# Kernel tuning notes

Hardware: AMD Instinct MI355X
Metric: run time of the kernel (lower is better)

## Reference

```python
import jax, jax.numpy as jnp
import numpy as np

D_MODEL = 1024
NHEAD = 16
HEAD_DIM = D_MODEL // NHEAD
EPS_NORM = 1e-6
EPS_RMS = 1e-6


def setup_inputs() -> dict:
    key = jax.random.key(0)
    ks = jax.random.split(key, 8)
    B, S = 2, 1024
    scale = 1.0 / np.sqrt(D_MODEL)
    x = jax.random.normal(ks[0], (B, S, D_MODEL), dtype=jnp.float32)
    Wq = jax.random.normal(ks[1], (D_MODEL, D_MODEL), dtype=jnp.float32) * scale
    Wk = jax.random.normal(ks[2], (D_MODEL, D_MODEL), dtype=jnp.float32) * scale
    Wv = jax.random.normal(ks[3], (D_MODEL, D_MODEL), dtype=jnp.float32) * scale
    Wb = jax.random.normal(ks[4], (NHEAD, D_MODEL), dtype=jnp.float32) * scale
    Wo = jax.random.normal(ks[5], (D_MODEL, D_MODEL), dtype=jnp.float32) * scale
    rms_w = jnp.ones((D_MODEL,), dtype=jnp.float32)
    return {"x": x, "Wq": Wq, "Wk": Wk, "Wv": Wv, "Wb": Wb, "Wo": Wo, "rms_w": rms_w}


def _l2_normalize(t):
    return t / (jnp.linalg.norm(t, axis=-1, keepdims=True) + EPS_NORM)


def _delta_forward(x, Wq, Wk, Wv, Wb, Wo, rms_w):
    B, S, dm = x.shape
    H, D = NHEAD, HEAD_DIM
    q = _l2_normalize(jax.nn.silu(x @ Wq.T).reshape(B, S, H, D))
    k = _l2_normalize(jax.nn.silu(x @ Wk.T).reshape(B, S, H, D))
    v = jax.nn.silu(x @ Wv.T).reshape(B, S, H, D)
    beta = jax.nn.sigmoid(x @ Wb.T) * 2.0  # (B,S,H), allow_neg_eigval doubles

    # time-major for scan: (S,B,H,D) / (S,B,H)
    qT = q.transpose(1, 0, 2, 3)
    kT = k.transpose(1, 0, 2, 3)
    vT = v.transpose(1, 0, 2, 3)
    bT = beta.transpose(1, 0, 2)

    def step(M, inp):
        qt, kt, vt, bt = inp
        # read state BEFORE update (strictly causal)
        out_t = jnp.einsum('bnh,bnhd->bnd', qt, M)
        retrieved = jnp.einsum('bnhd,bnd->bnh', M, kt)
        delta = vt - retrieved
        M = M + bt[..., None, None] * jnp.einsum('bnh,bnd->bnhd', kt, delta)
        return M, out_t

    M0 = jnp.zeros((B, H, D, D), dtype=x.dtype)
    _, outs = jax.lax.scan(step, M0, (qT, kT, vT, bT))  # (S,B,H,D)
    out = outs.transpose(1, 0, 2, 3).reshape(B, S, dm)

    # RMSNorm
    rms = jnp.sqrt(jnp.mean(out * out, axis=-1, keepdims=True) + EPS_RMS)
    out = out / rms * rms_w
    # output projection (dropout is identity in eval)
    return out @ Wo.T


def reference(x, Wq, Wk, Wv, Wb, Wo, rms_w):
    return _delta_forward(x, Wq, Wk, Wv, Wb, Wo, rms_w)
```

## Files before the change

kernel.cpp:

```cpp
#include <hip/hip_runtime.h>
#include <math.h>

#define D_MODEL 1024
#define NHEAD 16
#define HEAD_DIM 64
#define BATCH 2
#define SEQ 1024
#define ROWS (BATCH * SEQ)
#define RD (ROWS * D_MODEL)
#define WSZ (D_MODEL * D_MODEL)
#define CHUNK 64
#define NCHUNK (SEQ / CHUNK)

typedef __attribute__((ext_vector_type(8))) short bf16x8;
typedef __attribute__((ext_vector_type(8))) unsigned short ushort8;
typedef __attribute__((ext_vector_type(4))) unsigned short us4;
typedef __attribute__((ext_vector_type(4))) float f32x4;
typedef __attribute__((ext_vector_type(4))) unsigned int uint4v;
typedef unsigned short ushort;

__device__ __forceinline__ void load_lds_16u(const unsigned short* g, unsigned short* l) {
    __builtin_amdgcn_global_load_lds((const __attribute__((address_space(1))) void*)g,
                                     (__attribute__((address_space(3))) void*)l, 16, 0, 0);
}
__device__ __forceinline__ unsigned short f2bf(float x) {
    unsigned int u = __float_as_uint(x);
    unsigned int r = (u + 0x7FFFu + ((u >> 16) & 1u)) >> 16;
    return (unsigned short)r;
}
__device__ __forceinline__ float bf2f(unsigned short h) {
    return __uint_as_float(((unsigned int)h) << 16);
}
__device__ __forceinline__ float lane_bcast(float v, int lane) {
    return __uint_as_float(__builtin_amdgcn_readlane(__float_as_uint(v), lane));
}
#define SUBST 512
#define FBUF (8 * SUBST * 2)
__device__ __forceinline__ int fidx(int r, int k) {
    return ((r >> 4) * 2 + (k >> 5)) * SUBST + ((((k & 31) >> 3) << 4) + (r & 15)) * 8 + (k & 7);
}

__global__ __launch_bounds__(256) void split_kernel(const float* __restrict__ X,
                                                    unsigned short* __restrict__ H,
                                                    unsigned short* __restrict__ L,
                                                    int n4) {
    int i = blockIdx.x * 256 + threadIdx.x;
    if (i >= n4) return;
    float4 v = ((const float4*)X)[i];
    us4 h, l;
    h.x = f2bf(v.x); l.x = f2bf(v.x - bf2f(h.x));
    h.y = f2bf(v.y); l.y = f2bf(v.y - bf2f(h.y));
    h.z = f2bf(v.z); l.z = f2bf(v.z - bf2f(h.z));
    h.w = f2bf(v.w); l.w = f2bf(v.w - bf2f(h.w));
    ((us4*)H)[i] = h;
    ((us4*)L)[i] = l;
}

__global__ __launch_bounds__(256) void split3_kernel(const float* __restrict__ W0,
                                                     const float* __restrict__ W1,
                                                     const float* __restrict__ W2,
                                                     unsigned short* __restrict__ H0,
                                                     unsigned short* __restrict__ L0,
                                                     unsigned short* __restrict__ H1,
                                                     unsigned short* __restrict__ L1,
                                                     unsigned short* __restrict__ H2,
                                                     unsigned short* __restrict__ L2) {
    const int n4 = WSZ / 4;
    int i = blockIdx.x * 256 + threadIdx.x;
    const int which = i / n4;
    const int j = i - which * n4;
    const float* X = (which == 0) ? W0 : (which == 1) ? W1 : W2;
    unsigned short* H = (which == 0) ? H0 : (which == 1) ? H1 : H2;
    unsigned short* L = (which == 0) ? L0 : (which == 1) ? L1 : L2;
    float4 v = ((const float4*)X)[j];
    us4 h, l;
    h.x = f2bf(v.x); l.x = f2bf(v.x - bf2f(h.x));
    h.y = f2bf(v.y); l.y = f2bf(v.y - bf2f(h.y));
    h.z = f2bf(v.z); l.z = f2bf(v.z - bf2f(h.z));
    h.w = f2bf(v.w); l.w = f2bf(v.w - bf2f(h.w));
    ((us4*)H)[j] = h;
    ((us4*)L)[j] = l;
}

template <int ACT>
__device__ __forceinline__ void gemm_core(const unsigned short* __restrict__ Ah,
                                          const unsigned short* __restrict__ Al,
                                          const unsigned short* __restrict__ Bh,
                                          const unsigned short* __restrict__ Bl,
                                          float* __restrict__ C,
                                          int M, int N, int K,
                                          unsigned short* LA0, unsigned short* LA1,
                                          unsigned short* LB0, unsigned short* LB1) {
    const int t = threadIdx.x;
    const int wave = t >> 6, lane = t & 63;
    const int wm = wave >> 1, wn = wave & 1;
    const int m16 = lane & 15, kg = lane >> 4;
    const int row0 = blockIdx.y * 128, col0 = blockIdx.x * 64;

    f32x4 acc[4][2];
#pragma unroll
    for (int i = 0; i < 4; ++i)
#pragma unroll
        for (int j = 0; j < 2; ++j) acc[i][j] = (f32x4){0.f, 0.f, 0.f, 0.f};

    for (int k0 = 0; k0 < K; k0 += 32) {
#pragma unroll
        for (int ci = 0; ci < 6; ++ci) {
            const int c = wave * 6 + ci;
            const unsigned short* src;
            unsigned short* dst;
            int g16, rbase;
            if (c < 8)       { src = Ah; dst = &LA0[c * 512];        g16 = c;      rbase = row0; }
            else if (c < 16) { src = Al; dst = &LA1[(c - 8) * 512];  g16 = c - 8;  rbase = row0; }
            else if (c < 20) { src = Bh; dst = &LB0[(c - 16) * 512]; g16 = c - 16; rbase = col0; }
            else             { src = Bl; dst = &LB1[(c - 20) * 512]; g16 = c - 20; rbase = col0; }
            const unsigned short* gp = src + (size_t)(rbase + g16 * 16 + m16) * K + k0 + kg * 8;
            load_lds_16u(gp, dst);
        }
        __syncthreads();

        bf16x8 fah[4], fal[4], fbh[2], fbl[2];
#pragma unroll
        for (int mt = 0; mt < 4; ++mt) {
            const int off = (wm * 4 + mt) * 512 + lane * 8;
            fah[mt] = *(const bf16x8*)&LA0[off];
            fal[mt] = *(const bf16x8*)&LA1[off];
        }
#pragma unroll
        for (int nt = 0; nt < 2; ++nt) {
            const int off = (wn * 2 + nt) * 512 + lane * 8;
            fbh[nt] = *(const bf16x8*)&LB0[off];
            fbl[nt] = *(const bf16x8*)&LB1[off];
        }
#pragma unroll
        for (int mt = 0; mt < 4; ++mt)
#pragma unroll
            for (int nt = 0; nt < 2; ++nt) {
                acc[mt][nt] = __builtin_amdgcn_mfma_f32_16x16x32_bf16(fal[mt], fbh[nt], acc[mt][nt], 0, 0, 0);
                acc[mt][nt] = __builtin_amdgcn_mfma_f32_16x16x32_bf16(fah[mt], fbl[nt], acc[mt][nt], 0, 0, 0);
                acc[mt][nt] = __builtin_amdgcn_mfma_f32_16x16x32_bf16(fah[mt], fbh[nt], acc[mt][nt], 0, 0, 0);
            }
        __syncthreads();
    }

#pragma unroll
    for (int mt = 0; mt < 4; ++mt)
#pragma unroll
        for (int nt = 0; nt < 2; ++nt) {
            const int rowb = row0 + wm * 64 + mt * 16 + kg * 4;
            const int col  = col0 + wn * 32 + nt * 16 + m16;
#pragma unroll
            for (int rg = 0; rg < 4; ++rg) {
                float v = acc[mt][nt][rg];
                if (ACT == 1) v = v / (1.f + expf(-v));
                C[(size_t)(rowb + rg) * N + col] = v;
            }
        }
}

template <int ACT>
__global__ __launch_bounds__(256) void gemm_bf16s(const unsigned short* __restrict__ Ah,
                                                  const unsigned short* __restrict__ Al,
                                                  const unsigned short* __restrict__ Bh,
                                                  const unsigned short* __restrict__ Bl,
                                                  float* __restrict__ C,
                                                  int M, int N, int K) {
    __shared__ unsigned short LA[2][8 * 512];
    __shared__ unsigned short LB[2][4 * 512];
    gemm_core<ACT>(Ah, Al, Bh, Bl, C, M, N, K, LA[0], LA[1], LB[0], LB[1]);
}

__global__ __launch_bounds__(256) void gemm_qkv(const unsigned short* __restrict__ Ah,
                                                const unsigned short* __restrict__ Al,
                                                const unsigned short* __restrict__ Bqh,
                                                const unsigned short* __restrict__ Bql,
                                                const unsigned short* __restrict__ Bkh,
                                                const unsigned short* __restrict__ Bkl,
                                                const unsigned short* __restrict__ Bvh,
                                                const unsigned short* __restrict__ Bvl,
                                                float* __restrict__ Cq,
                                                float* __restrict__ Ck,
                                                float* __restrict__ Cv) {
    __shared__ unsigned short LA[2][8 * 512];
    __shared__ unsigned short LB[2][4 * 512];
    const int z = blockIdx.z;
    const unsigned short* Bh = (z == 0) ? Bqh : (z == 1) ? Bkh : Bvh;
    const unsigned short* Bl = (z == 0) ? Bql : (z == 1) ? Bkl : Bvl;
    float* C = (z == 0) ? Cq : (z == 1) ? Ck : Cv;
    gemm_core<1>(Ah, Al, Bh, Bl, C, ROWS, D_MODEL, D_MODEL, LA[0], LA[1], LB[0], LB[1]);
}

#define LDST 40
template <int ACT>
__global__ __launch_bounds__(256) void gemm_mfma(const float* __restrict__ A,
                                                 const float* __restrict__ B,
                                                 float* __restrict__ C,
                                                 int M, int N, int K) {
    __shared__ unsigned short Ahi[128 * LDST], Alo[128 * LDST];
    __shared__ unsigned short Bhi[128 * LDST], Blo[128 * LDST];

    const int t = threadIdx.x;
    const int wave = t >> 6, lane = t & 63;
    const int wm = wave >> 1, wn = wave & 1;
    const int row0 = blockIdx.y * 128, col0 = blockIdx.x * 128;
    const int sr = t >> 1;
    const int sh = t & 1;
    const int m16 = lane & 15, kg = lane >> 4;

    f32x4 acc[4][4];
#pragma unroll
    for (int i = 0; i < 4; ++i)
#pragma unroll
        for (int j = 0; j < 4; ++j) acc[i][j] = (f32x4){0.f, 0.f, 0.f, 0.f};

    const float* ga = A + (size_t)(row0 + sr) * K + sh * 16;
    const float* gb = B + (size_t)(col0 + sr) * K + sh * 16;
    const int sbase = sr * LDST + sh * 16;

    for (int k0 = 0; k0 < K; k0 += 32) {
        float af[16], bf[16];
#pragma unroll
        for (int i = 0; i < 4; ++i) {
            float4 a4 = *(const float4*)(ga + k0 + i * 4);
            float4 b4 = *(const float4*)(gb + k0 + i * 4);
            af[i * 4 + 0] = a4.x; af[i * 4 + 1] = a4.y; af[i * 4 + 2] = a4.z; af[i * 4 + 3] = a4.w;
            bf[i * 4 + 0] = b4.x; bf[i * 4 + 1] = b4.y; bf[i * 4 + 2] = b4.z; bf[i * 4 + 3] = b4.w;
        }
        ushort8 ah0, ah1, al0, al1, bh0, bh1, bl0, bl1;
#pragma unroll
        for (int j = 0; j < 8; ++j) {
            unsigned short h = f2bf(af[j]);       ah0[j] = h; al0[j] = f2bf(af[j] - bf2f(h));
            h = f2bf(af[j + 8]);                  ah1[j] = h; al1[j] = f2bf(af[j + 8] - bf2f(h));
            h = f2bf(bf[j]);                      bh0[j] = h; bl0[j] = f2bf(bf[j] - bf2f(h));
            h = f2bf(bf[j + 8]);                  bh1[j] = h; bl1[j] = f2bf(bf[j + 8] - bf2f(h));
        }
        *(ushort8*)&Ahi[sbase] = ah0;  *(ushort8*)&Ahi[sbase + 8] = ah1;
        *(ushort8*)&Alo[sbase] = al0;  *(ushort8*)&Alo[sbase + 8] = al1;
        *(ushort8*)&Bhi[sbase] = bh0;  *(ushort8*)&Bhi[sbase + 8] = bh1;
        *(ushort8*)&Blo[sbase] = bl0;  *(ushort8*)&Blo[sbase + 8] = bl1;
        __syncthreads();

        bf16x8 fah[4], fal[4], fbh[4], fbl[4];
#pragma unroll
        for (int i = 0; i < 4; ++i) {
            const int ar = (wm * 64 + i * 16 + m16) * LDST + kg * 8;
            const int br = (wn * 64 + i * 16 + m16) * LDST + kg * 8;
            fah[i] = *(const bf16x8*)&Ahi[ar];
            fal[i] = *(const bf16x8*)&Alo[ar];
            fbh[i] = *(const bf16x8*)&Bhi[br];
            fbl[i] = *(const bf16x8*)&Blo[br];
        }
#pragma unroll
        for (int i = 0; i < 4; ++i)
#pragma unroll
            for (int j = 0; j < 4; ++j) {
                acc[i][j] = __builtin_amdgcn_mfma_f32_16x16x32_bf16(fal[i], fbh[j], acc[i][j], 0, 0, 0);
                acc[i][j] = __builtin_amdgcn_mfma_f32_16x16x32_bf16(fah[i], fbl[j], acc[i][j], 0, 0, 0);
                acc[i][j] = __builtin_amdgcn_mfma_f32_16x16x32_bf16(fah[i], fbh[j], acc[i][j], 0, 0, 0);
            }
        __syncthreads();
    }

#pragma unroll
    for (int i = 0; i < 4; ++i)
#pragma unroll
        for (int j = 0; j < 4; ++j) {
            const int col = col0 + wn * 64 + j * 16 + m16;
            const int rowb = row0 + wm * 64 + i * 16 + kg * 4;
#pragma unroll
            for (int rg = 0; rg < 4; ++rg) {
                float v = acc[i][j][rg];
                if (ACT == 1) v = v / (1.f + expf(-v));
                C[(size_t)(rowb + rg) * N + col] = v;
            }
        }
}

__global__ __launch_bounds__(256) void beta_kernel(const float* __restrict__ x,
                                                   const float* __restrict__ Wb,
                                                   float* __restrict__ beta) {
    const int wave = blockIdx.x * 4 + (threadIdx.x >> 6);
    const int lane = threadIdx.x & 63;
    const float* xr = x + (size_t)wave * D_MODEL;
    float xv[16];
#pragma unroll
    for (int j = 0; j < 16; ++j) xv[j] = xr[lane + 64 * j];
    for (int n = 0; n < NHEAD; ++n) {
        const float* wr = Wb + (size_t)n * D_MODEL;
        float s = 0.f;
#pragma unroll
        for (int j = 0; j < 16; ++j) s += xv[j] * wr[lane + 64 * j];
#pragma unroll
        for (int off = 32; off; off >>= 1) s += __shfl_xor(s, off);
        if (lane == 0) beta[(size_t)wave * NHEAD + n] = 2.f / (1.f + expf(-s));
    }
}

__global__ __launch_bounds__(256) void norm_qk(float* __restrict__ Q,
                                               float* __restrict__ Kp) {
    const int TOT = ROWS * NHEAD;
    int wave = blockIdx.x * 4 + (threadIdx.x >> 6);
    const int lane = threadIdx.x & 63;
    float* T = (wave < TOT) ? Q : Kp;
    int w = (wave < TOT) ? wave : wave - TOT;
    float* p = T + (size_t)(w >> 4) * D_MODEL + (size_t)(w & 15) * HEAD_DIM;
    float v = p[lane];
    float ss = v * v;
#pragma unroll
    for (int off = 32; off; off >>= 1) ss += __shfl_xor(ss, off);
    p[lane] = v / (sqrtf(ss) + 1e-6f);
}

#define SMEM_SCAN 153088

__global__ __launch_bounds__(512, 1) void scan_chunked(const float* __restrict__ Qg,
                                                       const float* __restrict__ Kg,
                                                       const float* __restrict__ Vg,
                                                       const float* __restrict__ Btg,
                                                       float* __restrict__ Yg) {
    extern __shared__ char smem[];
    ushort* Mh_  = (ushort*)(smem + 0 * FBUF);
    ushort* Ml_  = (ushort*)(smem + 1 * FBUF);
    ushort* MTh_ = (ushort*)(smem + 2 * FBUF);
    ushort* MTl_ = (ushort*)(smem + 3 * FBUF);
    ushort* KTh_ = (ushort*)(smem + 4 * FBUF);
    ushort* KTl_ = (ushort*)(smem + 5 * FBUF);
    ushort* V0h_ = (ushort*)(smem + 6 * FBUF);
    ushort* V0l_ = (ushort*)(smem + 7 * FBUF);
    ushort* Gh_  = (ushort*)(smem + 8 * FBUF);
    ushort* Gl_  = (ushort*)(smem + 9 * FBUF);
    ushort* Kh_  = (ushort*)(smem + 10 * FBUF);
    ushort* Kl_  = (ushort*)(smem + 11 * FBUF);
    ushort* DTh_ = Kh_;
    ushort* DTl_ = Kl_;
    ushort* Qh_  = (ushort*)(smem + 12 * FBUF);
    ushort* Ql_  = (ushort*)(smem + 13 * FBUF);
    ushort* Wh_  = Qh_;
    ushort* Wl_  = Ql_;
    float*  V32  = (float*)(smem + 14 * FBUF);
    float*  C032 = V32;
    ushort* Ah_  = (ushort*)(smem + 14 * FBUF + 17408);
    ushort* Al_  = (ushort*)(smem + 15 * FBUF + 17408);
    float*  N32  = (float*)(smem + 16 * FBUF + 17408);
    float*  bv   = (float*)(smem + 16 * FBUF + 17408 + 4352);

    const int b = blockIdx.x >> 4;
    const int n = blockIdx.x & 15;
    const int t = threadIdx.x;
    const int wave = t >> 6, lane = t & 63;
    const int wm = wave >> 1, wn = wave & 1;
    const int m16 = lane & 15, kg = lane >> 4;
    const int bS = b * SEQ;
    const int nOff = n * HEAD_DIM;
    const int r = t >> 3, g = t & 7;

    f32x4 Macc[2], MTacc[2];
#pragma unroll
    for (int j = 0; j < 2; ++j) {
        Macc[j] = (f32x4){0.f, 0.f, 0.f, 0.f};
        MTacc[j] = (f32x4){0.f, 0.f, 0.f, 0.f};
    }

    auto prod_band = [&](const ushort* Ah, const ushort* Al,
                         const ushort* Bh, const ushort* Bl, f32x4 acc[2]) {
        const int lo8 = lane * 8;
#pragma unroll
        for (int half = 0; half < 2; ++half) {
            bf16x8 ah = *(const bf16x8*)&Ah[(wm * 2 + half) * SUBST + lo8];
            bf16x8 al = *(const bf16x8*)&Al[(wm * 2 + half) * SUBST + lo8];
#pragma unroll
            for (int j = 0; j < 2; ++j) {
                const int jg = wn * 2 + j;
                bf16x8 bh = *(const bf16x8*)&Bh[(jg * 2 + half) * SUBST + lo8];
                bf16x8 bl = *(const bf16x8*)&Bl[(jg * 2 + half) * SUBST + lo8];
                acc[j] = __builtin_amdgcn_mfma_f32_16x16x32_bf16(al, bh, acc[j], 0, 0, 0);
                acc[j] = __builtin_amdgcn_mfma_f32_16x16x32_bf16(ah, bl, acc[j], 0, 0, 0);
                acc[j] = __builtin_amdgcn_mfma_f32_16x16x32_bf16(ah, bh, acc[j], 0, 0, 0);
            }
        }
    };

    for (int c = 0; c < NCHUNK; ++c) {
        const int s0 = c * CHUNK;

        {
            const float* gK = Kg + (size_t)(bS + s0 + r) * D_MODEL + nOff + g * 8;
            const float* gQ = Qg + (size_t)(bS + s0 + r) * D_MODEL + nOff + g * 8;
            const float* gV = Vg + (size_t)(bS + s0 + r) * D_MODEL + nOff + g * 8;
            float kf[8], qf[8];
            ushort khv[8], klv[8];
            float4 kv0 = ((const float4*)gK)[0], kv1 = ((const float4*)gK)[1];
            float4 qv0 = ((const float4*)gQ)[0], qv1 = ((const float4*)gQ)[1];
            float4 vv0 = ((const float4*)gV)[0], vv1 = ((const float4*)gV)[1];
            kf[0] = kv0.x; kf[1] = kv0.y; kf[2] = kv0.z; kf[3] = kv0.w;
            kf[4] = kv1.x; kf[5] = kv1.y; kf[6] = kv1.z; kf[7] = kv1.w;
            qf[0] = qv0.x; qf[1] = qv0.y; qf[2] = qv0.z; qf[3] = qv0.w;
            qf[4] = qv1.x; qf[5] = qv1.y; qf[6] = qv1.z; qf[7] = qv1.w;
            *(float4*)&V32[r * 68 + g * 8] = vv0;
            *(float4*)&V32[r * 68 + g * 8 + 4] = vv1;
            ushort8 kh8, kl8, qh8, ql8;
#pragma unroll
            for (int e = 0; e < 8; ++e) {
                ushort h = f2bf(kf[e]);
                ushort l = f2bf(kf[e] - bf2f(h));
                khv[e] = h; klv[e] = l;
                kh8[e] = h; kl8[e] = l;
                h = f2bf(qf[e]); l = f2bf(qf[e] - bf2f(h));
                qh8[e] = h; ql8[e] = l;
            }
            const int o0 = fidx(r, g * 8);
            *(ushort8*)&Kh_[o0] = kh8;
            *(ushort8*)&Kl_[o0] = kl8;
            *(ushort8*)&Qh_[o0] = qh8;
            *(ushort8*)&Ql_[o0] = ql8;
#pragma unroll
            for (int e = 0; e < 8; ++e) {
                const int ib = fidx(g * 8 + e, r);
                KTh_[ib] = khv[e]; KTl_[ib] = klv[e];
            }
            if (t < 64) bv[t] = Btg[(size_t)(bS + s0 + t) * NHEAD + n];
        }
        __syncthreads();

        f32x4 yacc[2], V0acc[2];
        {
            if (c > 0) {
#pragma unroll
                for (int j = 0; j < 2; ++j) V0acc[j] = (f32x4){0.f, 0.f, 0.f, 0.f};
                prod_band(Kh_, Kl_, Mh_, Ml_, V0acc);
#pragma unroll
                for (int j = 0; j < 2; ++j)
#pragma unroll
                    for (int rg = 0; rg < 4; ++rg) {
                        const int row = wm * 16 + kg * 4 + rg, col = wn * 32 + j * 16 + m16;
                        V0acc[j][rg] = V32[row * 68 + col] - V0acc[j][rg];
                    }
            } else {
#pragma unroll
                for (int j = 0; j < 2; ++j)
#pragma unroll
                    for (int rg = 0; rg < 4; ++rg) {
                        const int row = wm * 16 + kg * 4 + rg, col = wn * 32 + j * 16 + m16;
                        V0acc[j][rg] = V32[row * 68 + col];
                    }
            }
#pragma unroll
            for (int j = 0; j < 2; ++j)
#pragma unroll
                for (int rg = 0; rg < 4; ++rg) {
                    const int row = wm * 16 + kg * 4 + rg, col = wn * 32 + j * 16 + m16;
                    float v0 = V0acc[j][rg];
                    ushort h = f2bf(v0);
                    const int ii = fidx(row, col);
                    V0h_[ii] = h; V0l_[ii] = f2bf(v0 - bf2f(h));
                }
#pragma unroll
            for (int j = 0; j < 2; ++j) yacc[j] = (f32x4){0.f, 0.f, 0.f, 0.f};
            if (c > 0) prod_band(Qh_, Ql_, MTh_, MTl_, yacc);
            f32x4 acc[2];
#pragma unroll
            for (int j = 0; j < 2; ++j) acc[j] = (f32x4){0.f, 0.f, 0.f, 0.f};
            prod_band(Kh_, Kl_, Kh_, Kl_, acc);
#pragma unroll
            for (int j = 0; j < 2; ++j)
#pragma unroll
                for (int rg = 0; rg < 4; ++rg) {
                    const int row = wm * 16 + kg * 4 + rg, col = wn * 32 + j * 16 + m16;
                    float av = acc[j][rg];
                    ushort h = f2bf(av);
                    const int ii = fidx(row, col);
                    Ah_[ii] = h; Al_[ii] = f2bf(av - bf2f(h));
                }
#pragma unroll
            for (int j = 0; j < 2; ++j) acc[j] = (f32x4){0.f, 0.f, 0.f, 0.f};
            prod_band(Qh_, Ql_, Kh_, Kl_, acc);
#pragma unroll
            for (int j = 0; j < 2; ++j)
#pragma unroll
                for (int rg = 0; rg < 4; ++rg) {
                    const int row = wm * 16 + kg * 4 + rg, col = wn * 32 + j * 16 + m16;
                    float gv = (row > col) ? acc[j][rg] : 0.f;
                    ushort h = f2bf(gv);
                    const int ii = fidx(row, col);
                    Gh_[ii] = h; Gl_[ii] = f2bf(gv - bf2f(h));
                }
        }
        __syncthreads();

        {
            f32x4 acc[2];
#pragma unroll
            for (int j = 0; j < 2; ++j) acc[j] = (f32x4){0.f, 0.f, 0.f, 0.f};
            prod_band(Kh_, Kl_, V0h_, V0l_, acc);
#pragma unroll
            for (int j = 0; j < 2; ++j)
#pragma unroll
                for (int rg = 0; rg < 4; ++rg) {
                    const int row = wm * 16 + kg * 4 + rg, col = wn * 32 + j * 16 + m16;
                    C032[row * 65 + col] = acc[j][rg];
                }
            for (int i = t; i < 2 * FBUF / 16; i += 512)
                ((uint4v*)Wh_)[i] = (uint4v){0u, 0u, 0u, 0u};
        }
        __syncthreads();

        if (wave == 0) {
#pragma unroll
            for (int J = 0; J < 4; ++J) {
                float Nreg[16];
                if (J > 0) {
#pragma unroll
                    for (int band = 0; band < 4; ++band) {
                        f32x4 acc1 = (f32x4){0.f, 0.f, 0.f, 0.f};
                        const int lo8 = lane * 8;
#pragma unroll
                        for (int half = 0; half < 2; ++half) {
                            bf16x8 ah = *(const bf16x8*)&Ah_[(band * 2 + half) * SUBST + lo8];
                            bf16x8 al = *(const bf16x8*)&Al_[(band * 2 + half) * SUBST + lo8];
                            bf16x8 bh = *(const bf16x8*)&Wh_[(J * 2 + half) * SUBST + lo8];
                            bf16x8 bl = *(const bf16x8*)&Wl_[(J * 2 + half) * SUBST + lo8];
                            acc1 = __builtin_amdgcn_mfma_f32_16x16x32_bf16(al, bh, acc1, 0, 0, 0);
                            acc1 = __builtin_amdgcn_mfma_f32_16x16x32_bf16(ah, bl, acc1, 0, 0, 0);
                            acc1 = __builtin_amdgcn_mfma_f32_16x16x32_bf16(ah, bh, acc1, 0, 0, 0);
                        }
#pragma unroll
                        for (int rg = 0; rg < 4; ++rg)
                            N32[(band * 16 + kg * 4 + rg) * 17 + m16] = acc1[rg];
                    }
#pragma unroll
                    for (int j = 0; j < 16; ++j) Nreg[j] = N32[lane * 17 + j];
                }

                float Areg[16], CNreg[16];
                {
                    bf16x8 a0 = *(const bf16x8*)&Ah_[fidx(lane, 16 * J)];
                    bf16x8 a1 = *(const bf16x8*)&Ah_[fidx(lane, 16 * J + 8)];
                    bf16x8 b0 = *(const bf16x8*)&Al_[fidx(lane, 16 * J)];
                    bf16x8 b1 = *(const bf16x8*)&Al_[fidx(lane, 16 * J + 8)];
#pragma unroll
                    for (int e = 0; e < 8; ++e) {
                        Areg[e]     = bf2f((ushort)a0[e]) + bf2f((ushort)b0[e]);
                        Areg[e + 8] = bf2f((ushort)a1[e]) + bf2f((ushort)b1[e]);
                    }
#pragma unroll
                    for (int j = 0; j < 16; ++j) CNreg[j] = C032[lane * 65 + 16 * J + j];
                    if (J > 0) {
#pragma unroll
                        for (int j = 0; j < 16; ++j) CNreg[j] += Nreg[j];
                    }
                }
                float bvreg = bv[16 * J + m16];

                float wreg[16];
#pragma unroll
                for (int j = 0; j < 16; ++j) {
                    float sA = CNreg[j], sB = 0.f;
#pragma unroll
                    for (int jj = 0; jj < 16; ++jj) {
                        if (jj < j) {
                            float pr = Areg[jj] * lane_bcast(wreg[jj], 16 * J + j);
                            if (jj & 1) sB += pr; else sA += pr;
                        }
                    }
                    float sum = sA + sB;
                    float beta_s = lane_bcast(bvreg, j);
                    wreg[j] = (lane > 16 * J + j) ? (-beta_s * sum) : 0.f;
                }

                {
                    ushort8 h8[2], l8[2];
#pragma unroll
                    for (int e = 0; e < 16; ++e) {
                        ushort h = f2bf(wreg[e]);
                        h8[e >> 3][e & 7] = h;
                        l8[e >> 3][e & 7] = f2bf(wreg[e] - bf2f(h));
                    }
                    const int o0 = fidx(lane, 16 * J), o1 = fidx(lane, 16 * J + 8);
                    *(ushort8*)&Wh_[o0] = h8[0]; *(ushort8*)&Wh_[o1] = h8[1];
                    *(ushort8*)&Wl_[o0] = l8[0]; *(ushort8*)&Wl_[o1] = l8[1];
                }
            }
        }
        __syncthreads();

        {
            f32x4 acc[2];
#pragma unroll
            for (int j = 0; j < 2; ++j) acc[j] = V0acc[j];
            prod_band(Wh_, Wl_, KTh_, KTl_, acc);
#pragma unroll
            for (int j = 0; j < 2; ++j)
#pragma unroll
                for (int rg = 0; rg < 4; ++rg) {
                    const int row = wm * 16 + kg * 4 + rg, col = wn * 32 + j * 16 + m16;
                    float dv = acc[j][rg] * bv[row];
                    ushort h = f2bf(dv);
                    const int ii = fidx(col, row);
                    DTh_[ii] = h; DTl_[ii] = f2bf(dv - bf2f(h));
                }
        }
        __syncthreads();

        {
            prod_band(Gh_, Gl_, DTh_, DTl_, yacc);
#pragma unroll
            for (int j = 0; j < 2; ++j)
#pragma unroll
                for (int rg = 0; rg < 4; ++rg) {
                    const int row = wm * 16 + kg * 4 + rg, col = wn * 32 + j * 16 + m16;
                    Yg[(size_t)(bS + s0 + row) * D_MODEL + nOff + col] = yacc[j][rg];
                }
            prod_band(KTh_, KTl_, DTh_, DTl_, Macc);
            prod_band(DTh_, DTl_, KTh_, KTl_, MTacc);
            if (c < NCHUNK - 1) {
#pragma unroll
                for (int j = 0; j < 2; ++j)
#pragma unroll
                    for (int rg = 0; rg < 4; ++rg) {
                        const int row = wm * 16 + kg * 4 + rg, col = wn * 32 + j * 16 + m16;
                        const int ii = fidx(row, col);
                        float mv = Macc[j][rg];
                        ushort h = f2bf(mv);
                        Mh_[ii] = h; Ml_[ii] = f2bf(mv - bf2f(h));
                        mv = MTacc[j][rg];
                        h = f2bf(mv);
                        MTh_[ii] = h; MTl_[ii] = f2bf(mv - bf2f(h));
                    }
            }
        }
        __syncthreads();
    }
}

template <int SPLIT>
__global__ __launch_bounds__(256) void rmsnorm_kernel(float* __restrict__ Y,
                                                      const float* __restrict__ w,
                                                      unsigned short* __restrict__ H,
                                                      unsigned short* __restrict__ L) {
    __shared__ float red[4];
    float* y = Y + (size_t)blockIdx.x * D_MODEL;
    const int t = threadIdx.x;
    const int wv = t >> 6, ln = t & 63;
    float4 v = ((float4*)y)[t];
    float ss = v.x * v.x + v.y * v.y + v.z * v.z + v.w * v.w;
#pragma unroll
    for (int off = 32; off; off >>= 1) ss += __shfl_xor(ss, off);
    if (ln == 0) red[wv] = ss;
    __syncthreads();
    float tot = red[0] + red[1] + red[2] + red[3];
    float inv = 1.f / sqrtf(tot * (1.f / D_MODEL) + 1e-6f);
    const float4 wv4 = ((const float4*)w)[t];
    v.x *= inv * wv4.x; v.y *= inv * wv4.y;
    v.z *= inv * wv4.z; v.w *= inv * wv4.w;
    if (SPLIT) {
        us4 h, l;
        h.x = f2bf(v.x); l.x = f2bf(v.x - bf2f(h.x));
        h.y = f2bf(v.y); l.y = f2bf(v.y - bf2f(h.y));
        h.z = f2bf(v.z); l.z = f2bf(v.z - bf2f(h.z));
        h.w = f2bf(v.w); l.w = f2bf(v.w - bf2f(h.w));
        size_t i = (size_t)blockIdx.x * 256 + t;
        ((us4*)H)[i] = h;
        ((us4*)L)[i] = l;
    } else {
        ((float4*)y)[t] = v;
    }
}

extern "C" void kernel_launch(void* const* d_in, const int* in_sizes, int n_in,
                              void* d_out, int out_size, void* d_ws, size_t ws_size,
                              hipStream_t stream) {
    const float* x     = (const float*)d_in[0];
    const float* Wq    = (const float*)d_in[1];
    const float* Wk    = (const float*)d_in[2];
    const float* Wv    = (const float*)d_in[3];
    const float* Wb    = (const float*)d_in[4];
    const float* Wo    = (const float*)d_in[5];
    const float* rms_w = (const float*)d_in[6];
    float* out = (float*)d_out;

    char* p = (char*)d_ws;
    float* Q  = (float*)p;  p += (size_t)RD * 4;
    float* Kp = (float*)p;  p += (size_t)RD * 4;
    float* Vp = (float*)p;  p += (size_t)RD * 4;
    float* Y  = (float*)p;  p += (size_t)RD * 4;
    float* Bt = (float*)p;  p += (size_t)32768 * 4;
    unsigned short* xh  = (unsigned short*)p;  p += (size_t)RD * 2;
    unsigned short* xl  = (unsigned short*)p;  p += (size_t)RD * 2;
    unsigned short* Wsh = (unsigned short*)p;  p += (size_t)WSZ * 2;
    unsigned short* Wsl = (unsigned short*)p;  p += (size_t)WSZ * 2;
    const size_t need_fast = (size_t)RD * 16 + 131072 + (size_t)RD * 4 + (size_t)WSZ * 4;
    const bool fast = ws_size >= need_fast;

    unsigned short* Wkh = (unsigned short*)Y;
    unsigned short* Wkl = Wkh + WSZ;
    unsigned short* Wvh = Wkl + WSZ;
    unsigned short* Wvl = Wvh + WSZ;

    (void)hipFuncSetAttribute(reinterpret_cast<const void*>(scan_chunked),
                              hipFuncAttributeMaxDynamicSharedMemorySize, SMEM_SCAN);

    if (fast) {
        dim3 ggrid(D_MODEL / 64, ROWS / 128);
        dim3 qgrid(D_MODEL / 64, ROWS / 128, 3);
        split_kernel<<<RD / 4 / 256, 256, 0, stream>>>(x, xh, xl, RD / 4);
        split3_kernel<<<3 * WSZ / 4 / 256, 256, 0, stream>>>(Wq, Wk, Wv,
                                                             Wsh, Wsl, Wkh, Wkl, Wvh, Wvl);
        gemm_qkv<<<qgrid, 256, 0, stream>>>(xh, xl, Wsh, Wsl, Wkh, Wkl, Wvh, Wvl,
                                            Q, Kp, Vp);
        beta_kernel<<<ROWS / 4, 256, 0, stream>>>(x, Wb, Bt);
        norm_qk<<<2 * ROWS * NHEAD / 4, 256, 0, stream>>>(Q, Kp);
        scan_chunked<<<BATCH * NHEAD, 512, SMEM_SCAN, stream>>>(Q, Kp, Vp, Bt, Y);
        rmsnorm_kernel<1><<<ROWS, 256, 0, stream>>>(Y, rms_w, xh, xl);
        split_kernel<<<WSZ / 4 / 256, 256, 0, stream>>>(Wo, Wsh, Wsl, WSZ / 4);
        gemm_bf16s<0><<<ggrid, 256, 0, stream>>>(xh, xl, Wsh, Wsl, out, ROWS, D_MODEL, D_MODEL);
    } else {
        dim3 ggrid(D_MODEL / 128, ROWS / 128);
        gemm_mfma<1><<<ggrid, 256, 0, stream>>>(x, Wq, Q, ROWS, D_MODEL, D_MODEL);
        gemm_mfma<1><<<ggrid, 256, 0, stream>>>(x, Wk, Kp, ROWS, D_MODEL, D_MODEL);
        gemm_mfma<1><<<ggrid, 256, 0, stream>>>(x, Wv, Vp, ROWS, D_MODEL, D_MODEL);
        beta_kernel<<<ROWS / 4, 256, 0, stream>>>(x, Wb, Bt);
        norm_qk<<<2 * ROWS * NHEAD / 4, 256, 0, stream>>>(Q, Kp);
        scan_chunked<<<BATCH * NHEAD, 512, SMEM_SCAN, stream>>>(Q, Kp, Vp, Bt, Y);
        rmsnorm_kernel<0><<<ROWS, 256, 0, stream>>>(Y, rms_w, nullptr, nullptr);
        gemm_mfma<0><<<ggrid, 256, 0, stream>>>(Y, Wo, out, ROWS, D_MODEL, D_MODEL);
    }
}
```

Measured before the change: 445.0 us.

## Overlap Q/G products with serial W solve and prefetch next chunk

Restructures the chunked delta-rule scan. Waves 1-7 now compute the Q·M^T and the causal Q·K^T (G) tiles while wave 0 does the serial triangular W solve, skipping G tiles that are entirely masked. The next chunk's K/Q/V are prefetched into registers, beta for the whole sequence is loaded once, and the MT state is written as the transpose of M instead of running a second MFMA product. The K A-fragments are reused across products. The cost is more registers and uneven per-wave work.

```diff
diff --git a/kernel.cpp b/kernel.cpp
--- a/kernel.cpp
+++ b/kernel.cpp
@@ -311,7 +311,7 @@
     p[lane] = v / (sqrtf(ss) + 1e-6f);
 }
 
-#define SMEM_SCAN 153088
+#define SMEM_SCAN 156160
 
 __global__ __launch_bounds__(512, 1) void scan_chunked(const float* __restrict__ Qg,
                                                        const float* __restrict__ Kg,
@@ -327,6 +327,8 @@
     ushort* KTl_ = (ushort*)(smem + 5 * FBUF);
     ushort* V0h_ = (ushort*)(smem + 6 * FBUF);
     ushort* V0l_ = (ushort*)(smem + 7 * FBUF);
+    ushort* Wh_  = V0h_;
+    ushort* Wl_  = V0l_;
     ushort* Gh_  = (ushort*)(smem + 8 * FBUF);
     ushort* Gl_  = (ushort*)(smem + 9 * FBUF);
     ushort* Kh_  = (ushort*)(smem + 10 * FBUF);
@@ -335,14 +337,11 @@
     ushort* DTl_ = Kl_;
     ushort* Qh_  = (ushort*)(smem + 12 * FBUF);
     ushort* Ql_  = (ushort*)(smem + 13 * FBUF);
-    ushort* Wh_  = Qh_;
-    ushort* Wl_  = Ql_;
-    float*  V32  = (float*)(smem + 14 * FBUF);
-    float*  C032 = V32;
-    ushort* Ah_  = (ushort*)(smem + 14 * FBUF + 17408);
-    ushort* Al_  = (ushort*)(smem + 15 * FBUF + 17408);
-    float*  N32  = (float*)(smem + 16 * FBUF + 17408);
-    float*  bv   = (float*)(smem + 16 * FBUF + 17408 + 4352);
+    float*  C032 = (float*)(smem + 14 * FBUF);
+    ushort* Ah_  = (ushort*)(smem + 14 * FBUF + 16640);
+    ushort* Al_  = (ushort*)(smem + 15 * FBUF + 16640);
+    float*  N32  = (float*)(smem + 16 * FBUF + 16640);
+    float*  bAll = (float*)(smem + 16 * FBUF + 16640 + 4352);
 
     const int b = blockIdx.x >> 4;
     const int n = blockIdx.x & 15;
@@ -354,51 +353,62 @@
     const int nOff = n * HEAD_DIM;
     const int r = t >> 3, g = t & 7;
 
-    f32x4 Macc[2], MTacc[2];
-#pragma unroll
-    for (int j = 0; j < 2; ++j) {
-        Macc[j] = (f32x4){0.f, 0.f, 0.f, 0.f};
-        MTacc[j] = (f32x4){0.f, 0.f, 0.f, 0.f};
-    }
-
-    auto prod_band = [&](const ushort* Ah, const ushort* Al,
-                         const ushort* Bh, const ushort* Bl, f32x4 acc[2]) {
+    f32x4 Macc[2];
+    Macc[0] = (f32x4){0.f, 0.f, 0.f, 0.f};
+    Macc[1] = (f32x4){0.f, 0.f, 0.f, 0.f};
+
+    auto load_af = [&](const ushort* Xh, const ushort* Xl, int tm, bf16x8* oh, bf16x8* ol) {
         const int lo8 = lane * 8;
 #pragma unroll
         for (int half = 0; half < 2; ++half) {
-            bf16x8 ah = *(const bf16x8*)&Ah[(wm * 2 + half) * SUBST + lo8];
-            bf16x8 al = *(const bf16x8*)&Al[(wm * 2 + half) * SUBST + lo8];
+            oh[half] = *(const bf16x8*)&Xh[(tm * 2 + half) * SUBST + lo8];
+            ol[half] = *(const bf16x8*)&Xl[(tm * 2 + half) * SUBST + lo8];
+        }
+    };
+    auto prod_cA = [&](const bf16x8* ah, const bf16x8* al,
+                       const ushort* Bh, const ushort* Bl, int tn, f32x4* acc) {
+        const int lo8 = lane * 8;
+#pragma unroll
+        for (int half = 0; half < 2; ++half) {
 #pragma unroll
             for (int j = 0; j < 2; ++j) {
-                const int jg = wn * 2 + j;
+                const int jg = tn * 2 + j;
                 bf16x8 bh = *(const bf16x8*)&Bh[(jg * 2 + half) * SUBST + lo8];
                 bf16x8 bl = *(const bf16x8*)&Bl[(jg * 2 + half) * SUBST + lo8];
-                acc[j] = __builtin_amdgcn_mfma_f32_16x16x32_bf16(al, bh, acc[j], 0, 0, 0);
-                acc[j] = __builtin_amdgcn_mfma_f32_16x16x32_bf16(ah, bl, acc[j], 0, 0, 0);
-                acc[j] = __builtin_amdgcn_mfma_f32_16x16x32_bf16(ah, bh, acc[j], 0, 0, 0);
+                acc[j] = __builtin_amdgcn_mfma_f32_16x16x32_bf16(al[half], bh, acc[j], 0, 0, 0);
+                acc[j] = __builtin_amdgcn_mfma_f32_16x16x32_bf16(ah[half], bl, acc[j], 0, 0, 0);
+                acc[j] = __builtin_amdgcn_mfma_f32_16x16x32_bf16(ah[half], bh, acc[j], 0, 0, 0);
             }
         }
     };
+
+    for (int i = t; i < SEQ; i += 512) bAll[i] = Btg[(size_t)(bS + i) * NHEAD + n];
+
+    float4 pk0, pk1, pq0, pq1;
+    float pv[8];
+    auto issue_pf = [&](int cc) {
+        const int so = cc * CHUNK;
+        const float* gK = Kg + (size_t)(bS + so + r) * D_MODEL + nOff + g * 8;
+        const float* gQ = Qg + (size_t)(bS + so + r) * D_MODEL + nOff + g * 8;
+        pk0 = ((const float4*)gK)[0]; pk1 = ((const float4*)gK)[1];
+        pq0 = ((const float4*)gQ)[0]; pq1 = ((const float4*)gQ)[1];
+        const float* gV = Vg + (size_t)(bS + so) * D_MODEL + nOff;
+#pragma unroll
+        for (int j = 0; j < 2; ++j)
+#pragma unroll
+            for (int rg = 0; rg < 4; ++rg)
+                pv[j * 4 + rg] = gV[(size_t)(wm * 16 + kg * 4 + rg) * D_MODEL + wn * 32 + j * 16 + m16];
+    };
+    issue_pf(0);
 
     for (int c = 0; c < NCHUNK; ++c) {
         const int s0 = c * CHUNK;
 
         {
-            const float* gK = Kg + (size_t)(bS + s0 + r) * D_MODEL + nOff + g * 8;
-            const float* gQ = Qg + (size_t)(bS + s0 + r) * D_MODEL + nOff + g * 8;
-            const float* gV = Vg + (size_t)(bS + s0 + r) * D_MODEL + nOff + g * 8;
-            float kf[8], qf[8];
+            float kf[8] = {pk0.x, pk0.y, pk0.z, pk0.w, pk1.x, pk1.y, pk1.z, pk1.w};
+            float qf[8] = {pq0.x, pq0.y, pq0.z, pq0.w, pq1.x, pq1.y, pq1.z, pq1.w};
+            ushort8 kh8, kl8, qh8, ql8;
             ushort khv[8], klv[8];
-            float4 kv0 = ((const float4*)gK)[0], kv1 = ((const float4*)gK)[1];
-            float4 qv0 = ((const float4*)gQ)[0], qv1 = ((const float4*)gQ)[1];
-            float4 vv0 = ((const float4*)gV)[0], vv1 = ((const float4*)gV)[1];
-            kf[0] = kv0.x; kf[1] = kv0.y; kf[2] = kv0.z; kf[3] = kv0.w;
-            kf[4] = kv1.x; kf[5] = kv1.y; kf[6] = kv1.z; kf[7] = kv1.w;
-            qf[0] = qv0.x; qf[1] = qv0.y; qf[2] = qv0.z; qf[3] = qv0.w;
-            qf[4] = qv1.x; qf[5] = qv1.y; qf[6] = qv1.z; qf[7] = qv1.w;
-            *(float4*)&V32[r * 68 + g * 8] = vv0;
-            *(float4*)&V32[r * 68 + g * 8 + 4] = vv1;
-            ushort8 kh8, kl8, qh8, ql8;
 #pragma unroll
             for (int e = 0; e < 8; ++e) {
                 ushort h = f2bf(kf[e]);
@@ -418,93 +428,72 @@
                 const int ib = fidx(g * 8 + e, r);
                 KTh_[ib] = khv[e]; KTl_[ib] = klv[e];
             }
-            if (t < 64) bv[t] = Btg[(size_t)(bS + s0 + t) * NHEAD + n];
-        }
-        __syncthreads();
-
-        f32x4 yacc[2], V0acc[2];
+        }
+        __syncthreads();
+
+        bf16x8 kah[2], kal[2];
+        f32x4 V0acc[2];
         {
-            if (c > 0) {
-#pragma unroll
-                for (int j = 0; j < 2; ++j) V0acc[j] = (f32x4){0.f, 0.f, 0.f, 0.f};
-                prod_band(Kh_, Kl_, Mh_, Ml_, V0acc);
-#pragma unroll
-                for (int j = 0; j < 2; ++j)
-#pragma unroll
-                    for (int rg = 0; rg < 4; ++rg) {
-                        const int row = wm * 16 + kg * 4 + rg, col = wn * 32 + j * 16 + m16;
-                        V0acc[j][rg] = V32[row * 68 + col] - V0acc[j][rg];
-                    }
-            } else {
-#pragma unroll
-                for (int j = 0; j < 2; ++j)
-#pragma unroll
-                    for (int rg = 0; rg < 4; ++rg) {
-                        const int row = wm * 16 + kg * 4 + rg, col = wn * 32 + j * 16 + m16;
-                        V0acc[j][rg] = V32[row * 68 + col];
-                    }
-            }
+            load_af(Kh_, Kl_, wm, kah, kal);
+            V0acc[0] = (f32x4){0.f, 0.f, 0.f, 0.f};
+            V0acc[1] = (f32x4){0.f, 0.f, 0.f, 0.f};
+            if (c > 0) prod_cA(kah, kal, Mh_, Ml_, wn, V0acc);
+#pragma unroll
+            for (int j = 0; j < 2; ++j)
+#pragma unroll
+                for (int rg = 0; rg < 4; ++rg)
+                    V0acc[j][rg] = pv[j * 4 + rg] - V0acc[j][rg];
 #pragma unroll
             for (int j = 0; j < 2; ++j)
 #pragma unroll
                 for (int rg = 0; rg < 4; ++rg) {
                     const int row = wm * 16 + kg * 4 + rg, col = wn * 32 + j * 16 + m16;
-                    float v0 = V0acc[j][rg];
-                    ushort h = f2bf(v0);
+                    const float v0 = V0acc[j][rg];
+                    const ushort h = f2bf(v0);
                     const int ii = fidx(row, col);
                     V0h_[ii] = h; V0l_[ii] = f2bf(v0 - bf2f(h));
                 }
-#pragma unroll
-            for (int j = 0; j < 2; ++j) yacc[j] = (f32x4){0.f, 0.f, 0.f, 0.f};
-            if (c > 0) prod_band(Qh_, Ql_, MTh_, MTl_, yacc);
-            f32x4 acc[2];
-#pragma unroll
-            for (int j = 0; j < 2; ++j) acc[j] = (f32x4){0.f, 0.f, 0.f, 0.f};
-            prod_band(Kh_, Kl_, Kh_, Kl_, acc);
+            f32x4 aacc[2];
+            aacc[0] = (f32x4){0.f, 0.f, 0.f, 0.f};
+            aacc[1] = (f32x4){0.f, 0.f, 0.f, 0.f};
+            prod_cA(kah, kal, Kh_, Kl_, wn, aacc);
 #pragma unroll
             for (int j = 0; j < 2; ++j)
 #pragma unroll
                 for (int rg = 0; rg < 4; ++rg) {
                     const int row = wm * 16 + kg * 4 + rg, col = wn * 32 + j * 16 + m16;
-                    float av = acc[j][rg];
-                    ushort h = f2bf(av);
+                    const float av = aacc[j][rg];
+                    const ushort h = f2bf(av);
                     const int ii = fidx(row, col);
                     Ah_[ii] = h; Al_[ii] = f2bf(av - bf2f(h));
                 }
-#pragma unroll
-            for (int j = 0; j < 2; ++j) acc[j] = (f32x4){0.f, 0.f, 0.f, 0.f};
-            prod_band(Qh_, Ql_, Kh_, Kl_, acc);
+        }
+        __syncthreads();
+
+        {
+            f32x4 cacc[2];
+            cacc[0] = (f32x4){0.f, 0.f, 0.f, 0.f};
+            cacc[1] = (f32x4){0.f, 0.f, 0.f, 0.f};
+            prod_cA(kah, kal, V0h_, V0l_, wn, cacc);
 #pragma unroll
             for (int j = 0; j < 2; ++j)
 #pragma unroll
                 for (int rg = 0; rg < 4; ++rg) {
                     const int row = wm * 16 + kg * 4 + rg, col = wn * 32 + j * 16 + m16;
-                    float gv = (row > col) ? acc[j][rg] : 0.f;
-                    ushort h = f2bf(gv);
-                    const int ii = fidx(row, col);
-                    Gh_[ii] = h; Gl_[ii] = f2bf(gv - bf2f(h));
+                    C032[row * 65 + col] = cacc[j][rg];
                 }
         }
         __syncthreads();
 
-        {
-            f32x4 acc[2];
-#pragma unroll
-            for (int j = 0; j < 2; ++j) acc[j] = (f32x4){0.f, 0.f, 0.f, 0.f};
-            prod_band(Kh_, Kl_, V0h_, V0l_, acc);
-#pragma unroll
-            for (int j = 0; j < 2; ++j)
-#pragma unroll
-                for (int rg = 0; rg < 4; ++rg) {
-                    const int row = wm * 16 + kg * 4 + rg, col = wn * 32 + j * 16 + m16;
-                    C032[row * 65 + col] = acc[j][rg];
-                }
-            for (int i = t; i < 2 * FBUF / 16; i += 512)
-                ((uint4v*)Wh_)[i] = (uint4v){0u, 0u, 0u, 0u};
-        }
-        __syncthreads();
+        if (c + 1 < NCHUNK) issue_pf(c + 1);
+
+        f32x4 yacc[2][2];
 
         if (wave == 0) {
+#pragma unroll
+            for (int i0 = 0; i0 < 16; ++i0)
+                ((uint4v*)Wh_)[i0 * 64 + lane] = (uint4v){0u, 0u, 0u, 0u};
+
 #pragma unroll
             for (int J = 0; J < 4; ++J) {
                 float Nreg[16];
@@ -549,7 +538,7 @@
                         for (int j = 0; j < 16; ++j) CNreg[j] += Nreg[j];
                     }
                 }
-                float bvreg = bv[16 * J + m16];
+                float bvreg = bAll[s0 + 16 * J + m16];
 
                 float wreg[16];
 #pragma unroll
@@ -580,51 +569,93 @@
                     *(ushort8*)&Wl_[o0] = l8[0]; *(ushort8*)&Wl_[o1] = l8[1];
                 }
             }
+        } else {
+            const int nt_w = (wave == 4) ? 0 : ((wave <= 2) ? 2 : 1);
+            const int wi = (wave < 4) ? (wave - 1) : (wave - 2);
+#pragma unroll
+            for (int ti = 0; ti < 2; ++ti) {
+                if (ti >= nt_w) continue;
+                const int T = (ti == 0) ? wi : (wi + 6);
+                const int twm = T >> 1, twn = T & 1;
+                bf16x8 qh2[2], ql2[2];
+                load_af(Qh_, Ql_, twm, qh2, ql2);
+                yacc[ti][0] = (f32x4){0.f, 0.f, 0.f, 0.f};
+                yacc[ti][1] = (f32x4){0.f, 0.f, 0.f, 0.f};
+                if (c > 0) prod_cA(qh2, ql2, MTh_, MTl_, twn, yacc[ti]);
+                const bool gz = (twm * 16 + 15) <= (twn * 32);
+                f32x4 ga[2];
+                ga[0] = (f32x4){0.f, 0.f, 0.f, 0.f};
+                ga[1] = (f32x4){0.f, 0.f, 0.f, 0.f};
+                if (!gz) prod_cA(qh2, ql2, Kh_, Kl_, twn, ga);
+#pragma unroll
+                for (int j = 0; j < 2; ++j)
+#pragma unroll
+                    for (int rg = 0; rg < 4; ++rg) {
+                        const int row = twm * 16 + kg * 4 + rg, col = twn * 32 + j * 16 + m16;
+                        const float gv = (row > col) ? ga[j][rg] : 0.f;
+                        const ushort h = f2bf(gv);
+                        const int ii = fidx(row, col);
+                        Gh_[ii] = h; Gl_[ii] = f2bf(gv - bf2f(h));
+                    }
+            }
         }
         __syncthreads();
 
         {
-            f32x4 acc[2];
-#pragma unroll
-            for (int j = 0; j < 2; ++j) acc[j] = V0acc[j];
-            prod_band(Wh_, Wl_, KTh_, KTl_, acc);
+            f32x4 dacc[2];
+            dacc[0] = V0acc[0]; dacc[1] = V0acc[1];
+            bf16x8 wh2[2], wl2[2];
+            load_af(Wh_, Wl_, wm, wh2, wl2);
+            prod_cA(wh2, wl2, KTh_, KTl_, wn, dacc);
 #pragma unroll
             for (int j = 0; j < 2; ++j)
 #pragma unroll
                 for (int rg = 0; rg < 4; ++rg) {
                     const int row = wm * 16 + kg * 4 + rg, col = wn * 32 + j * 16 + m16;
-                    float dv = acc[j][rg] * bv[row];
-                    ushort h = f2bf(dv);
+                    const float dv = dacc[j][rg] * bAll[s0 + row];
+                    const ushort h = f2bf(dv);
                     const int ii = fidx(col, row);
                     DTh_[ii] = h; DTl_[ii] = f2bf(dv - bf2f(h));
                 }
         }
         __syncthreads();
 
+        if (wave != 0) {
+            const int nt_w = (wave == 4) ? 0 : ((wave <= 2) ? 2 : 1);
+            const int wi = (wave < 4) ? (wave - 1) : (wave - 2);
+#pragma unroll
+            for (int ti = 0; ti < 2; ++ti) {
+                if (ti >= nt_w) continue;
+                const int T = (ti == 0) ? wi : (wi + 6);
+                const int twm = T >> 1, twn = T & 1;
+                bf16x8 gh2[2], gl2[2];
+                load_af(Gh_, Gl_, twm, gh2, gl2);
+                prod_cA(gh2, gl2, DTh_, DTl_, twn, yacc[ti]);
+#pragma unroll
+                for (int j = 0; j < 2; ++j)
+#pragma unroll
+                    for (int rg = 0; rg < 4; ++rg) {
+                        const int row = twm * 16 + kg * 4 + rg, col = twn * 32 + j * 16 + m16;
+                        Yg[(size_t)(bS + s0 + row) * D_MODEL + nOff + col] = yacc[ti][j][rg];
+                    }
+            }
+        }
         {
-            prod_band(Gh_, Gl_, DTh_, DTl_, yacc);
-#pragma unroll
-            for (int j = 0; j < 2; ++j)
-#pragma unroll
-                for (int rg = 0; rg < 4; ++rg) {
-                    const int row = wm * 16 + kg * 4 + rg, col = wn * 32 + j * 16 + m16;
-                    Yg[(size_t)(bS + s0 + row) * D_MODEL + nOff + col] = yacc[j][rg];
-                }
-            prod_band(KTh_, KTl_, DTh_, DTl_, Macc);
-            prod_band(DTh_, DTl_, KTh_, KTl_, MTacc);
+            bf16x8 kth[2], ktl[2];
+            load_af(KTh_, KTl_, wm, kth, ktl);
+            prod_cA(kth, ktl, DTh_, DTl_, wn, Macc);
             if (c < NCHUNK - 1) {
 #pragma unroll
                 for (int j = 0; j < 2; ++j)
 #pragma unroll
                     for (int rg = 0; rg < 4; ++rg) {
                         const int row = wm * 16 + kg * 4 + rg, col = wn * 32 + j * 16 + m16;
+                        const float mv = Macc[j][rg];
+                        const ushort h = f2bf(mv), l = f2bf(mv - bf2f(h));
                         const int ii = fidx(row, col);
-                        float mv = Macc[j][rg];
-                        ushort h = f2bf(mv);
-                        Mh_[ii] = h; Ml_[ii] = f2bf(mv - bf2f(h));
-                        mv = MTacc[j][rg];
-                        h = f2bf(mv);
-                        MTh_[ii] = h; MTl_[ii] = f2bf(mv - bf2f(h));
+                        Mh_[ii] = h; Ml_[ii] = l;
+                        const int iT = fidx(col, row);
+                        MTh_[iT] = h; MTl_[iT] = l;
                     }
             }
         }
```

After: 442.0 us. Within noise of the previous version (-0.7%).
